# Kernel tuning notes

Hardware: AMD Instinct MI355X
Metric: run time of the kernel (lower is better)

The kernel has to match this reference:

```python
import jax, jax.numpy as jnp
import numpy as np

B, NPG, A, E = 128, 512, 8, 504   # graphs, nodes/graph, agents, edges/graph
F_IN, HID, H = 3, 64, 8
C = HID
F = H * C                          # 512 = concat head output
OUT = 2
NEG_SLOPE = 0.2


def _seg_softmax(alpha, dst, n):
    # edge-softmax normalized over destination-node neighborhoods
    m = jax.ops.segment_max(alpha, dst, num_segments=n)
    e = jnp.exp(alpha - m[dst])
    s = jax.ops.segment_sum(e, dst, num_segments=n)
    return e / jnp.clip(s[dst], 1e-16)


def _gat(x, src, dst, ea, W, b, a_s, a_d, We, a_e, n, self_loops):
    # PyG GATConv: heads=H, concat=True, edge_dim=1, fill_value='mean'
    xs = (x @ W).reshape(n, H, C)                      # [N,H,C]
    als = jnp.einsum('nhc,hc->nh', xs, a_s)            # alpha_src per node
    ald = jnp.einsum('nhc,hc->nh', xs, a_d)            # alpha_dst per node
    if self_loops:
        # fill_value='mean': self-loop attr = mean of incoming edge attrs
        ssum = jax.ops.segment_sum(ea, dst, num_segments=n)
        cnt = jax.ops.segment_sum(jnp.ones((dst.shape[0], 1), ea.dtype), dst, num_segments=n)
        loop_attr = ssum / jnp.maximum(cnt, 1.0)
        ea = jnp.concatenate([ea, loop_attr], axis=0)
        loop = jnp.arange(n, dtype=src.dtype)
        src = jnp.concatenate([src, loop])
        dst = jnp.concatenate([dst, loop])
    ee = (ea @ We).reshape(-1, H, C)                   # lin_edge
    ale = jnp.einsum('ehc,hc->eh', ee, a_e)            # alpha_edge per edge
    alpha = jax.nn.leaky_relu(als[src] + ald[dst] + ale, NEG_SLOPE)  # [E,H]
    alpha = _seg_softmax(alpha, dst, n)
    out = jax.ops.segment_sum(alpha[:, :, None] * xs[src], dst, num_segments=n)
    return out.reshape(n, H * C) + b


def _forward(x, edge_index, edge_attr, p1, p2, p3, fc1_w, fc1_b, fc2_w, fc2_b):
    Bq, npg, _ = x.shape
    n = Bq * npg
    off = (jnp.arange(Bq, dtype=edge_index.dtype) * npg)[:, None]   # PyG Batch offsets
    src = (edge_index[..., 0] + off).reshape(-1)
    dst = (edge_index[..., 1] + off).reshape(-1)
    ea = edge_attr.reshape(-1, 1)
    h = x.reshape(n, -1)
    h = jax.nn.relu(_gat(h, src, dst, ea, *p1, n, False))   # conv1: add_self_loops=False
    h = jax.nn.relu(_gat(h, src, dst, ea, *p2, n, True))
    h = jax.nn.relu(_gat(h, src, dst, ea, *p3, n, True))
    hg = h.reshape(Bq, npg, F)
    graph_emb = hg.mean(axis=1)                      # global_mean_pool (equal-size graphs)
    agent_emb = hg[:, :A].reshape(Bq * A, F)         # first num_agents nodes per graph
    comb = jnp.concatenate([agent_emb, jnp.repeat(graph_emb, A, axis=0)], axis=1)
    comb = jax.nn.relu(comb @ fc1_w + fc1_b)         # fc1 ReLU (extra torch.relu is idempotent)
    pred = comb @ fc2_w + fc2_b
    return pred.reshape(Bq, A, OUT)


def setup_inputs() -> dict:
    key = jax.random.key(0)
    ks = jax.random.split(key, 32)
    rn = lambda i, shape: jax.random.normal(ks[i], shape, jnp.float32) * 0.05
    inp = {
        'x': jax.random.normal(ks[0], (B, NPG, F_IN), jnp.float32),
        'edge_index': jax.random.randint(ks[1], (B, E, 2), 0, NPG, jnp.int32),
        'edge_attr': jax.random.normal(ks[2], (B, E, 1), jnp.float32),
    }
    dims = [F_IN, F, F]
    for li, din in enumerate(dims, start=1):
        inp[f'W{li}'] = rn(3 + li * 6, (din, H * C))
        inp[f'b{li}'] = jnp.zeros((H * C,), jnp.float32)
        inp[f'as{li}'] = rn(4 + li * 6, (H, C))
        inp[f'ad{li}'] = rn(5 + li * 6, (H, C))
        inp[f'We{li}'] = rn(6 + li * 6, (1, H * C))
        inp[f'ae{li}'] = rn(7 + li * 6, (H, C))
    inp['fc1_w'] = rn(28, (2 * F, 4 * HID))
    inp['fc1_b'] = jnp.zeros((4 * HID,), jnp.float32)
    inp['fc2_w'] = rn(29, (4 * HID, OUT))
    inp['fc2_b'] = jnp.zeros((OUT,), jnp.float32)
    return inp


def reference(x, edge_index, edge_attr,
              W1, b1, as1, ad1, We1, ae1,
              W2, b2, as2, ad2, We2, ae2,
              W3, b3, as3, ad3, We3, ae3,
              fc1_w, fc1_b, fc2_w, fc2_b):
    p1 = (W1, b1, as1, ad1, We1, ae1)
    p2 = (W2, b2, as2, ad2, We2, ae2)
    p3 = (W3, b3, as3, ad3, We3, ae3)
    return _forward(x, edge_index, edge_attr, p1, p2, p3, fc1_w, fc1_b, fc2_w, fc2_b)
```

## Files before the change

kernel.cpp:

```cpp
#include <hip/hip_runtime.h>
#include <hip/hip_bf16.h>
#include <math.h>

#define NGRAPH 128
#define NPG_   512
#define NN     (NGRAPH*NPG_)
#define EPG    504
#define ETOT   (NGRAPH*EPG)
#define HEADS  8
#define FDIM   512
#define NEG    0.2f

typedef __hip_bfloat16 bf16;
typedef __attribute__((ext_vector_type(8))) short short8;
typedef __attribute__((ext_vector_type(4))) float f32x4;

static __device__ __forceinline__ float bf(short s){
  union { unsigned u; float f; } c; c.u = ((unsigned)(unsigned short)s) << 16; return c.f;
}
static __device__ __forceinline__ short fbf(float v){
  bf16 b = __float2bfloat16(v); return *(short*)&b;
}

static __device__ __forceinline__ void gload16(void* lds, const void* g){
  __builtin_amdgcn_global_load_lds((const __attribute__((address_space(1))) void*)g,
                                   (__attribute__((address_space(3))) void*)lds, 16, 0, 0);
}

__global__ void k_sentinel(float* out, int n){
  int i = blockIdx.x*blockDim.x + threadIdx.x;
  if (i < n) out[i] = 12345.0f;
}

__global__ __launch_bounds__(512) void k_csr(const int* __restrict__ ei, const float* __restrict__ ea,
                                             const float* __restrict__ We0, const float* __restrict__ ae0,
                                             const float* __restrict__ We1, const float* __restrict__ ae1,
                                             const float* __restrict__ We2, const float* __restrict__ ae2,
                                             const float* __restrict__ W1,
                                             const float* __restrict__ as1, const float* __restrict__ ad1,
                                             int* __restrict__ deg_g, int* __restrict__ row_ptr,
                                             float* __restrict__ la,
                                             int* __restrict__ esrc, float* __restrict__ eattr,
                                             float* __restrict__ coef, float* __restrict__ wsd){
  int b = blockIdx.x;
  int t = threadIdx.x;
  if (b >= NGRAPH){
    if (b < NGRAPH+3){
      int l = b - NGRAPH;
      const float* We = l==0 ? We0 : (l==1 ? We1 : We2);
      const float* ae = l==0 ? ae0 : (l==1 ? ae1 : ae2);
      float v = We[t]*ae[t];
      #pragma unroll
      for (int o=32;o>0;o>>=1) v += __shfl_down(v, o);
      if ((t & 63) == 0) coef[l*HEADS + (t>>6)] = v;
      return;
    }
    float as_v = as1[t], ad_v = ad1[t];
    float v[6] = { W1[t]*as_v, W1[512+t]*as_v, W1[1024+t]*as_v,
                   W1[t]*ad_v, W1[512+t]*ad_v, W1[1024+t]*ad_v };
    #pragma unroll
    for (int o=32;o>0;o>>=1){
      #pragma unroll
      for (int q=0;q<6;q++) v[q] += __shfl_down(v[q], o);
    }
    if ((t & 63) == 0){
      int w = t >> 6;
      wsd[w*3+0]    = v[0]; wsd[w*3+1]    = v[1]; wsd[w*3+2]    = v[2];
      wsd[24+w*3+0] = v[3]; wsd[24+w*3+1] = v[4]; wsd[24+w*3+2] = v[5];
    }
    return;
  }
  __shared__ int   dg[512];
  __shared__ float ss[512];
  __shared__ int   scan[512];
  __shared__ int   cur[512];
  dg[t] = 0; ss[t] = 0.f;
  __syncthreads();
  int src=0, dst=0; float at=0.f;
  if (t < EPG){
    src = ei[(b*EPG+t)*2];
    dst = ei[(b*EPG+t)*2+1];
    at  = ea[b*EPG+t];
    atomicAdd(&dg[dst], 1);
    atomicAdd(&ss[dst], at);
  }
  __syncthreads();
  int d = dg[t];
  scan[t] = d;
  __syncthreads();
  for (int o=1;o<512;o<<=1){
    int v2 = (t>=o) ? scan[t-o] : 0;
    __syncthreads();
    scan[t] += v2;
    __syncthreads();
  }
  int excl = scan[t] - d;
  int n = b*NPG_ + t;
  row_ptr[n] = b*EPG + excl;
  deg_g[n]   = d;
  la[n]      = ss[t] / fmaxf((float)d, 1.f);
  cur[t] = excl;
  __syncthreads();
  if (t < EPG){
    int slot = atomicAdd(&cur[dst], 1);
    int p = b*EPG + slot;
    esrc[p]  = b*NPG_ + src;
    eattr[p] = at;
  }
}

__global__ void k_wt(const float* __restrict__ W1, const float* __restrict__ W2,
                     bf16* __restrict__ wt){
  int idx = blockIdx.x*blockDim.x + threadIdx.x;
  if (idx >= 2*FDIM*FDIM) return;
  int l = idx >> 18;
  int r = idx & (FDIM*FDIM-1);
  int n = r >> 9, k = r & 511;
  const float* W = l ? W2 : W1;
  wt[idx] = __float2bfloat16(W[k*FDIM + n]);
}

__global__ __launch_bounds__(256) void k_gat1(const float* __restrict__ x,
                                              const float* __restrict__ W,
                                              const float* __restrict__ wsd,
                                              const float* __restrict__ coef,
                                              const int* __restrict__ row_ptr,
                                              const int* __restrict__ deg,
                                              const int* __restrict__ esrc,
                                              const float* __restrict__ eattr,
                                              const float* __restrict__ bias,
                                              bf16* __restrict__ h){
  int nwg = gridDim.x;
  int cpx = nwg >> 3;
  int bid = blockIdx.x;
  int swz = (bid & 7)*cpx + (bid >> 3);
  int n = swz*4 + (threadIdx.x >> 6);
  int lane = threadIdx.x & 63;
  int hh = lane >> 3;
  int f0 = lane << 3;

  float ws0 = wsd[hh*3+0],    ws1 = wsd[hh*3+1],    ws2 = wsd[hh*3+2];
  float wd0 = wsd[24+hh*3+0], wd1 = wsd[24+hh*3+1], wd2 = wsd[24+hh*3+2];
  float ch = coef[hh];

  const float* xr = x + n*3;
  float aldn = xr[0]*wd0 + xr[1]*wd1 + xr[2]*wd2;

  int row = row_ptr[n], d = deg[n];
  float m = -1e30f, ssum = 0.f;
  float a0 = 0.f, a1 = 0.f, a2 = 0.f;
  for (int i=0;i<d;i++){
    int s = esrc[row+i]; float at = eattr[row+i];
    const float* xsr = x + s*3;
    float y0 = xsr[0], y1 = xsr[1], y2 = xsr[2];
    float raw = y0*ws0 + y1*ws1 + y2*ws2 + aldn + at*ch;
    raw = raw > 0.f ? raw : NEG*raw;
    float mn = fmaxf(m, raw);
    float sc = __expf(m - mn);
    float p  = __expf(raw - mn);
    ssum = ssum*sc + p;
    a0 = a0*sc + p*y0;
    a1 = a1*sc + p*y1;
    a2 = a2*sc + p*y2;
    m = mn;
  }
  float inv = 1.f / fmaxf(ssum, 1e-16f);
  a0 *= inv; a1 *= inv; a2 *= inv;

  float w0[8], w1[8], w2[8], b8[8];
  #pragma unroll
  for (int j=0;j<8;j+=4){
    *(float4*)&w0[j] = *(const float4*)&W[f0+j];
    *(float4*)&w1[j] = *(const float4*)&W[FDIM+f0+j];
    *(float4*)&w2[j] = *(const float4*)&W[2*FDIM+f0+j];
    *(float4*)&b8[j] = *(const float4*)&bias[f0+j];
  }
  short8 r;
  #pragma unroll
  for (int j=0;j<8;j++){
    float o = a0*w0[j] + a1*w1[j] + a2*w2[j] + b8[j];
    r[j] = fbf(o > 0.f ? o : 0.f);
  }
  ((short8*)(h + (size_t)n*FDIM))[lane] = r;
}

__global__ __launch_bounds__(256) void k_attn_node(const bf16* __restrict__ xs,
                                                   const float* __restrict__ a_s,
                                                   const float* __restrict__ a_d,
                                                   float* __restrict__ als,
                                                   float* __restrict__ ald){
  int n = blockIdx.x*4 + (threadIdx.x >> 6);
  int lane = threadIdx.x & 63;
  short8 v = ((const short8*)(xs + (size_t)n*FDIM))[lane];
  const float4* as4 = (const float4*)a_s;
  const float4* ad4 = (const float4*)a_d;
  float4 sa = as4[lane*2], sb = as4[lane*2+1];
  float4 da = ad4[lane*2], db = ad4[lane*2+1];
  float s = bf(v[0])*sa.x + bf(v[1])*sa.y + bf(v[2])*sa.z + bf(v[3])*sa.w
          + bf(v[4])*sb.x + bf(v[5])*sb.y + bf(v[6])*sb.z + bf(v[7])*sb.w;
  float d = bf(v[0])*da.x + bf(v[1])*da.y + bf(v[2])*da.z + bf(v[3])*da.w
          + bf(v[4])*db.x + bf(v[5])*db.y + bf(v[6])*db.z + bf(v[7])*db.w;
  #pragma unroll
  for (int o=1;o<8;o<<=1){ s += __shfl_xor(s, o); d += __shfl_xor(d, o); }
  if ((lane & 7) == 0){
    int hh = lane >> 3;
    als[n*HEADS+hh] = s;
    ald[n*HEADS+hh] = d;
  }
}

__global__ __launch_bounds__(256) void k_gat(const bf16* __restrict__ xs,
                                             const float* __restrict__ als,
                                             const float* __restrict__ ald,
                                             const float* __restrict__ coef,
                                             const int* __restrict__ row_ptr,
                                             const int* __restrict__ deg,
                                             const int* __restrict__ esrc,
                                             const float* __restrict__ eattr,
                                             const float* __restrict__ la,
                                             const float* __restrict__ bias,
                                             bf16* __restrict__ h){
  int nwg = gridDim.x;
  int cpx = nwg >> 3;
  int bid = blockIdx.x;
  int swz = (bid & 7)*cpx + (bid >> 3);
  int n = swz*4 + (threadIdx.x >> 6);
  int lane = threadIdx.x & 63;
  int hh = lane >> 3;
  int row = row_ptr[n], d = deg[n];
  int tot = d + 1;
  float aldn = ald[n*HEADS+hh];
  float ch = coef[hh];
  float lan = la[n];

  float m = -1e30f, ssum = 0.f;
  float acc[8] = {};
  for (int i=0;i<tot;i++){
    int s; float at;
    if (i<d){ s = esrc[row+i]; at = eattr[row+i]; }
    else    { s = n;           at = lan; }
    float raw = als[s*HEADS+hh] + aldn + at*ch;
    raw = raw > 0.f ? raw : NEG*raw;
    float mn = fmaxf(m, raw);
    float scale = __expf(m - mn);
    float p = __expf(raw - mn);
    ssum = ssum*scale + p;
    short8 v = ((const short8*)(xs + (size_t)s*FDIM))[lane];
    #pragma unroll
    for (int j=0;j<8;j++) acc[j] = acc[j]*scale + p*bf(v[j]);
    m = mn;
  }
  float inv = 1.f / fmaxf(ssum, 1e-16f);
  const float4* b4 = (const float4*)bias;
  float4 ba = b4[lane*2], bb = b4[lane*2+1];
  float bias8[8] = {ba.x,ba.y,ba.z,ba.w,bb.x,bb.y,bb.z,bb.w};
  short8 r;
  #pragma unroll
  for (int j=0;j<8;j++){
    float o = acc[j]*inv + bias8[j];
    r[j] = fbf(o > 0.f ? o : 0.f);
  }
  ((short8*)(h + (size_t)n*FDIM))[lane] = r;
}

__global__ __launch_bounds__(256) void gemm_mfma(const bf16* __restrict__ A,
                                                 const bf16* __restrict__ Wt,
                                                 bf16* __restrict__ C,
                                                 int M, int N, int K){
  __shared__ short As[128*64];
  __shared__ short Bs[128*64];
  int bid = blockIdx.x;
  int wk = ((bid & 7) << 8) | (bid >> 3);
  const int bm = (wk >> 2)*128, bn = (wk & 3)*128;
  const int tid = threadIdx.x;
  const int lane = tid & 63;
  const int w = tid >> 6;
  const int wm = (w >> 1)*64, wn = (w & 1)*64;
  const int lr = lane & 15;
  const int lk = lane >> 4;

  f32x4 acc[4][4] = {};

  for (int k0 = 0; k0 < K; k0 += 64){
    #pragma unroll
    for (int is = 0; is < 4; ++is){
      int i = is*256 + tid;
      int r = i >> 3, g = i & 7;
      int gs = g ^ (r & 7);
      gload16(&As[i*8], A  + (size_t)(bm+r)*K + k0 + gs*8);
      gload16(&Bs[i*8], Wt + (size_t)(bn+r)*K + k0 + gs*8);
    }
    __syncthreads();
    #pragma unroll
    for (int kk = 0; kk < 2; ++kk){
      short8 af[4], bfr[4];
      #pragma unroll
      for (int mi=0; mi<4; ++mi){
        int row = wm + mi*16 + lr;
        int g = (kk*4 + lk) ^ (row & 7);
        af[mi] = *(const short8*)&As[row*64 + g*8];
      }
      #pragma unroll
      for (int ni=0; ni<4; ++ni){
        int row = wn + ni*16 + lr;
        int g = (kk*4 + lk) ^ (row & 7);
        bfr[ni] = *(const short8*)&Bs[row*64 + g*8];
      }
      #pragma unroll
      for (int mi=0; mi<4; ++mi)
        #pragma unroll
        for (int ni=0; ni<4; ++ni)
          acc[mi][ni] = __builtin_amdgcn_mfma_f32_16x16x32_bf16(af[mi], bfr[ni], acc[mi][ni], 0,0,0);
    }
    __syncthreads();
  }

  #pragma unroll
  for (int mi=0; mi<4; ++mi)
    #pragma unroll
    for (int ni=0; ni<4; ++ni){
      int col = bn + wn + ni*16 + lr;
      #pragma unroll
      for (int r=0; r<4; ++r){
        int rowg = bm + wm + mi*16 + lk*4 + r;
        C[(size_t)rowg*N + col] = __float2bfloat16(acc[mi][ni][r]);
      }
    }
}

__global__ __launch_bounds__(256) void k_gemb1(const bf16* __restrict__ h, float* __restrict__ pgemb){
  int gs_ = blockIdx.x;
  int g = gs_ >> 3, s = gs_ & 7;
  int t = threadIdx.x;
  int c = t & 63, rg = t >> 6;
  const bf16* base = h + ((size_t)(g*NPG_ + s*64 + rg*16))*FDIM;
  float acc[8] = {};
  #pragma unroll 4
  for (int i=0;i<16;i++){
    short8 v = ((const short8*)(base + (size_t)i*FDIM))[c];
    #pragma unroll
    for (int j=0;j<8;j++) acc[j] += bf(v[j]);
  }
  float* dst = pgemb + ((size_t)(gs_*4 + rg))*FDIM + c*8;
  float4 lo = {acc[0],acc[1],acc[2],acc[3]};
  float4 hi = {acc[4],acc[5],acc[6],acc[7]};
  *(float4*)dst = lo;
  *(float4*)(dst+4) = hi;
}

__global__ __launch_bounds__(1024) void k_head(const bf16* __restrict__ h,
                                               const float* __restrict__ pgemb,
                                               const float* __restrict__ fc1w,
                                               const float* __restrict__ fc1b,
                                               const float* __restrict__ fc2w,
                                               const float* __restrict__ fc2b,
                                               float* __restrict__ out){
  __shared__ float ge[FDIM];
  __shared__ float ag[8][FDIM];
  __shared__ float ps[2][8][257];
  __shared__ float gs2[2][256];
  __shared__ float f1[8][256];
  int g = blockIdx.x, t = threadIdx.x;

  if (t < FDIM){
    float s = 0.f;
    const float* p = pgemb + (size_t)g*32*FDIM + t;
    #pragma unroll
    for (int c=0;c<32;c++) s += p[(size_t)c*FDIM];
    ge[t] = s * (1.f/NPG_);
  } else {
    int i = t - FDIM;
    int r = i >> 6, c = i & 63;
    short8 v = ((const short8*)(h + (size_t)(g*NPG_ + r)*FDIM))[c];
    #pragma unroll
    for (int j=0;j<8;j++) ag[r][c*8+j] = bf(v[j]);
  }
  __syncthreads();

  int col = t & 255, q = t >> 8;
  if (q < 2){
    float acc[8] = {};
    int kbeg = q*256;
    for (int k = kbeg; k < kbeg+256; k += 4){
      float w0 = fc1w[(k+0)*256+col];
      float w1 = fc1w[(k+1)*256+col];
      float w2 = fc1w[(k+2)*256+col];
      float w3 = fc1w[(k+3)*256+col];
      #pragma unroll
      for (int r=0;r<8;r++){
        float4 a = *(const float4*)&ag[r][k];
        acc[r] += a.x*w0 + a.y*w1 + a.z*w2 + a.w*w3;
      }
    }
    #pragma unroll
    for (int r=0;r<8;r++) ps[q][r][col] = acc[r];
  } else {
    float gacc = 0.f;
    int kbeg = (q-2)*256;
    for (int k = kbeg; k < kbeg+256; k += 4){
      float v0 = fc1w[(FDIM+k+0)*256+col];
      float v1 = fc1w[(FDIM+k+1)*256+col];
      float v2 = fc1w[(FDIM+k+2)*256+col];
      float v3 = fc1w[(FDIM+k+3)*256+col];
      float4 gv = *(const float4*)&ge[k];
      gacc += gv.x*v0 + gv.y*v1 + gv.z*v2 + gv.w*v3;
    }
    gs2[q-2][col] = gacc;
  }
  __syncthreads();

  if (t < 256){
    float b = fc1b[t] + gs2[0][t] + gs2[1][t];
    #pragma unroll
    for (int r=0;r<8;r++)
      f1[r][t] = fmaxf(ps[0][r][t] + ps[1][r][t] + b, 0.f);
  }
  __syncthreads();

  if (t < 128){
    int r = t >> 4, o = (t >> 3) & 1, l = t & 7;
    float s = 0.f;
    for (int k = l; k < 256; k += 8) s += f1[r][k] * fc2w[k*2+o];
    #pragma unroll
    for (int off=4; off; off>>=1) s += __shfl_down(s, off);
    if (l == 0) out[(g*8 + r)*2 + o] = s + fc2b[o];
  }
}

extern "C" void kernel_launch(void* const* d_in, const int* in_sizes, int n_in,
                              void* d_out, int out_size, void* d_ws, size_t ws_size,
                              hipStream_t stream)
{
  const float* x    = (const float*)d_in[0];
  const int*   ei   = (const int*)  d_in[1];
  const float* ea   = (const float*)d_in[2];
  const float* Wl[3]  = {(const float*)d_in[3],  (const float*)d_in[9],  (const float*)d_in[15]};
  const float* Bl[3]  = {(const float*)d_in[4],  (const float*)d_in[10], (const float*)d_in[16]};
  const float* ASl[3] = {(const float*)d_in[5],  (const float*)d_in[11], (const float*)d_in[17]};
  const float* ADl[3] = {(const float*)d_in[6],  (const float*)d_in[12], (const float*)d_in[18]};
  const float* WEl[3] = {(const float*)d_in[7],  (const float*)d_in[13], (const float*)d_in[19]};
  const float* AEl[3] = {(const float*)d_in[8],  (const float*)d_in[14], (const float*)d_in[20]};
  const float* FC1W = (const float*)d_in[21];
  const float* FC1B = (const float*)d_in[22];
  const float* FC2W = (const float*)d_in[23];
  const float* FC2B = (const float*)d_in[24];
  float* out = (float*)d_out;
  (void)in_sizes; (void)n_in;

  char* ws = (char*)d_ws;
  size_t off = 0;
  auto alloc = [&](size_t bytes)->char*{
    char* p = ws + off;
    off = (off + bytes + 255) & ~(size_t)255;
    return p;
  };
  bf16*  h       = (bf16*) alloc((size_t)NN*FDIM*2);
  bf16*  xs      = (bf16*) alloc((size_t)NN*FDIM*2);
  float* als     = (float*)alloc((size_t)NN*HEADS*4);
  float* ald     = (float*)alloc((size_t)NN*HEADS*4);
  float* la      = (float*)alloc((size_t)NN*4);
  int*   deg     = (int*)  alloc((size_t)NN*4);
  int*   row_ptr = (int*)  alloc((size_t)NN*4);
  int*   esrc    = (int*)  alloc((size_t)ETOT*4);
  float* eattr   = (float*)alloc((size_t)ETOT*4);
  float* coef    = (float*)alloc(3*HEADS*4);
  float* wsd     = (float*)alloc(48*4);
  bf16*  wt      = (bf16*) alloc((size_t)2*FDIM*FDIM*2);
  float* pgemb   = (float*)alloc((size_t)NGRAPH*32*FDIM*4);

  if (off > ws_size){
    k_sentinel<<<(out_size+255)/256, 256, 0, stream>>>(out, out_size);
    return;
  }

  k_csr<<<NGRAPH+4, 512, 0, stream>>>(ei, ea, WEl[0], AEl[0], WEl[1], AEl[1], WEl[2], AEl[2],
                                      Wl[0], ASl[0], ADl[0],
                                      deg, row_ptr, la, esrc, eattr, coef, wsd);
  k_wt<<<(2*FDIM*FDIM+255)/256, 256, 0, stream>>>(Wl[1], Wl[2], wt);

  k_gat1<<<NN/4, 256, 0, stream>>>(x, Wl[0], wsd, coef, row_ptr, deg, esrc, eattr, Bl[0], h);

  for (int l=1;l<3;l++){
    gemm_mfma<<<2048, 256, 0, stream>>>(h, wt + (size_t)(l-1)*FDIM*FDIM, xs, NN, FDIM, FDIM);
    k_attn_node<<<NN/4, 256, 0, stream>>>(xs, ASl[l], ADl[l], als, ald);
    k_gat<<<NN/4, 256, 0, stream>>>(xs, als, ald, coef + l*HEADS, row_ptr, deg, esrc, eattr, la, Bl[l], h);
  }

  k_gemb1<<<NGRAPH*8, 256, 0, stream>>>(h, pgemb);
  k_head <<<NGRAPH, 1024, 0, stream>>>(h, pgemb, FC1W, FC1B, FC2W, FC2B, out);
}
```

Before: 255.1 us.

## Fuse attention-score projection into GEMM epilogue and split head over K

The per-node attention dot products (alpha_src/alpha_dst) are now computed inside the MFMA GEMM epilogue from fp32 accumulators, which removes the separate k_attn_node kernel and its re-read of xs. Each 64-column wave tile maps to one head, so the reduction is a 16-lane shuffle. The readout head is split into a K-parallel k_head1 over 1024 blocks that writes partial sums, followed by a small k_fc2 reduction. This exposes more parallelism than 128 large blocks, at the cost of extra workspace traffic and a slightly different rounding (fp32 instead of bf16 xs for the scores).

```diff
diff --git a/kernel.cpp b/kernel.cpp
--- a/kernel.cpp
+++ b/kernel.cpp
@@ -182,31 +182,6 @@
     r[j] = fbf(o > 0.f ? o : 0.f);
   }
   ((short8*)(h + (size_t)n*FDIM))[lane] = r;
-}
-
-__global__ __launch_bounds__(256) void k_attn_node(const bf16* __restrict__ xs,
-                                                   const float* __restrict__ a_s,
-                                                   const float* __restrict__ a_d,
-                                                   float* __restrict__ als,
-                                                   float* __restrict__ ald){
-  int n = blockIdx.x*4 + (threadIdx.x >> 6);
-  int lane = threadIdx.x & 63;
-  short8 v = ((const short8*)(xs + (size_t)n*FDIM))[lane];
-  const float4* as4 = (const float4*)a_s;
-  const float4* ad4 = (const float4*)a_d;
-  float4 sa = as4[lane*2], sb = as4[lane*2+1];
-  float4 da = ad4[lane*2], db = ad4[lane*2+1];
-  float s = bf(v[0])*sa.x + bf(v[1])*sa.y + bf(v[2])*sa.z + bf(v[3])*sa.w
-          + bf(v[4])*sb.x + bf(v[5])*sb.y + bf(v[6])*sb.z + bf(v[7])*sb.w;
-  float d = bf(v[0])*da.x + bf(v[1])*da.y + bf(v[2])*da.z + bf(v[3])*da.w
-          + bf(v[4])*db.x + bf(v[5])*db.y + bf(v[6])*db.z + bf(v[7])*db.w;
-  #pragma unroll
-  for (int o=1;o<8;o<<=1){ s += __shfl_xor(s, o); d += __shfl_xor(d, o); }
-  if ((lane & 7) == 0){
-    int hh = lane >> 3;
-    als[n*HEADS+hh] = s;
-    ald[n*HEADS+hh] = d;
-  }
 }
 
 __global__ __launch_bounds__(256) void k_gat(const bf16* __restrict__ xs,
@@ -265,7 +240,11 @@
 
 __global__ __launch_bounds__(256) void gemm_mfma(const bf16* __restrict__ A,
                                                  const bf16* __restrict__ Wt,
+                                                 const float* __restrict__ a_s,
+                                                 const float* __restrict__ a_d,
                                                  bf16* __restrict__ C,
+                                                 float* __restrict__ als,
+                                                 float* __restrict__ ald,
                                                  int M, int N, int K){
   __shared__ short As[128*64];
   __shared__ short Bs[128*64];
@@ -315,6 +294,31 @@
     __syncthreads();
   }
 
+  int hh = (bn + wn) >> 6;
+  float as_c[4], ad_c[4];
+  #pragma unroll
+  for (int ni=0; ni<4; ++ni){
+    int c = hh*64 + ni*16 + lr;
+    as_c[ni] = a_s[c];
+    ad_c[ni] = a_d[c];
+  }
+  #pragma unroll
+  for (int mi=0; mi<4; ++mi)
+    #pragma unroll
+    for (int r=0; r<4; ++r){
+      float s = acc[mi][0][r]*as_c[0] + acc[mi][1][r]*as_c[1]
+              + acc[mi][2][r]*as_c[2] + acc[mi][3][r]*as_c[3];
+      float d = acc[mi][0][r]*ad_c[0] + acc[mi][1][r]*ad_c[1]
+              + acc[mi][2][r]*ad_c[2] + acc[mi][3][r]*ad_c[3];
+      #pragma unroll
+      for (int o=1;o<16;o<<=1){ s += __shfl_xor(s, o); d += __shfl_xor(d, o); }
+      if (lr == 0){
+        int rowg = bm + wm + mi*16 + lk*4 + r;
+        als[rowg*HEADS+hh] = s;
+        ald[rowg*HEADS+hh] = d;
+      }
+    }
+
   #pragma unroll
   for (int mi=0; mi<4; ++mi)
     #pragma unroll
@@ -348,75 +352,67 @@
   *(float4*)(dst+4) = hi;
 }
 
-__global__ __launch_bounds__(1024) void k_head(const bf16* __restrict__ h,
+__global__ __launch_bounds__(256) void k_head1(const bf16* __restrict__ h,
                                                const float* __restrict__ pgemb,
                                                const float* __restrict__ fc1w,
-                                               const float* __restrict__ fc1b,
-                                               const float* __restrict__ fc2w,
-                                               const float* __restrict__ fc2b,
-                                               float* __restrict__ out){
-  __shared__ float ge[FDIM];
-  __shared__ float ag[8][FDIM];
-  __shared__ float ps[2][8][257];
-  __shared__ float gs2[2][256];
+                                               float* __restrict__ pf1,
+                                               float* __restrict__ pge){
+  __shared__ float ge[64];
+  __shared__ float ag[8][64];
+  int blk = blockIdx.x;
+  int g = blk >> 3, q = blk & 7;
+  int t = threadIdx.x;
+  int k0 = q*64;
+
+  if (t < 64){
+    float s = 0.f;
+    const float* p = pgemb + ((size_t)g*32)*FDIM + k0 + t;
+    #pragma unroll 8
+    for (int c=0;c<32;c++) s += p[(size_t)c*FDIM];
+    ge[t] = s * (1.f/NPG_);
+  } else if (t < 128){
+    int i = t - 64;
+    int r = i >> 3, c8 = i & 7;
+    short8 v = ((const short8*)(h + ((size_t)(g*NPG_ + r))*FDIM + k0))[c8];
+    #pragma unroll
+    for (int j=0;j<8;j++) ag[r][c8*8+j] = bf(v[j]);
+  }
+  __syncthreads();
+
+  float acc[8] = {};
+  float gacc = 0.f;
+  for (int kk=0; kk<64; kk++){
+    float wa = fc1w[(size_t)(k0+kk)*256 + t];
+    float wg = fc1w[(size_t)(FDIM+k0+kk)*256 + t];
+    #pragma unroll
+    for (int r=0;r<8;r++) acc[r] += ag[r][kk]*wa;
+    gacc += ge[kk]*wg;
+  }
+  #pragma unroll
+  for (int r=0;r<8;r++) pf1[((size_t)q*1024 + g*8 + r)*256 + t] = acc[r];
+  pge[((size_t)q*NGRAPH + g)*256 + t] = gacc;
+}
+
+__global__ __launch_bounds__(256) void k_fc2(const float* __restrict__ pf1,
+                                             const float* __restrict__ pge,
+                                             const float* __restrict__ fc1b,
+                                             const float* __restrict__ fc2w,
+                                             const float* __restrict__ fc2b,
+                                             float* __restrict__ out){
   __shared__ float f1[8][256];
   int g = blockIdx.x, t = threadIdx.x;
-
-  if (t < FDIM){
+  float ges = 0.f;
+  #pragma unroll
+  for (int q=0;q<8;q++) ges += pge[((size_t)q*NGRAPH + g)*256 + t];
+  float b = fc1b[t] + ges;
+  #pragma unroll
+  for (int r=0;r<8;r++){
     float s = 0.f;
-    const float* p = pgemb + (size_t)g*32*FDIM + t;
-    #pragma unroll
-    for (int c=0;c<32;c++) s += p[(size_t)c*FDIM];
-    ge[t] = s * (1.f/NPG_);
-  } else {
-    int i = t - FDIM;
-    int r = i >> 6, c = i & 63;
-    short8 v = ((const short8*)(h + (size_t)(g*NPG_ + r)*FDIM))[c];
-    #pragma unroll
-    for (int j=0;j<8;j++) ag[r][c*8+j] = bf(v[j]);
-  }
-  __syncthreads();
-
-  int col = t & 255, q = t >> 8;
-  if (q < 2){
-    float acc[8] = {};
-    int kbeg = q*256;
-    for (int k = kbeg; k < kbeg+256; k += 4){
-      float w0 = fc1w[(k+0)*256+col];
-      float w1 = fc1w[(k+1)*256+col];
-      float w2 = fc1w[(k+2)*256+col];
-      float w3 = fc1w[(k+3)*256+col];
-      #pragma unroll
-      for (int r=0;r<8;r++){
-        float4 a = *(const float4*)&ag[r][k];
-        acc[r] += a.x*w0 + a.y*w1 + a.z*w2 + a.w*w3;
-      }
-    }
-    #pragma unroll
-    for (int r=0;r<8;r++) ps[q][r][col] = acc[r];
-  } else {
-    float gacc = 0.f;
-    int kbeg = (q-2)*256;
-    for (int k = kbeg; k < kbeg+256; k += 4){
-      float v0 = fc1w[(FDIM+k+0)*256+col];
-      float v1 = fc1w[(FDIM+k+1)*256+col];
-      float v2 = fc1w[(FDIM+k+2)*256+col];
-      float v3 = fc1w[(FDIM+k+3)*256+col];
-      float4 gv = *(const float4*)&ge[k];
-      gacc += gv.x*v0 + gv.y*v1 + gv.z*v2 + gv.w*v3;
-    }
-    gs2[q-2][col] = gacc;
-  }
-  __syncthreads();
-
-  if (t < 256){
-    float b = fc1b[t] + gs2[0][t] + gs2[1][t];
-    #pragma unroll
-    for (int r=0;r<8;r++)
-      f1[r][t] = fmaxf(ps[0][r][t] + ps[1][r][t] + b, 0.f);
-  }
-  __syncthreads();
-
+    #pragma unroll
+    for (int q=0;q<8;q++) s += pf1[((size_t)q*1024 + g*8 + r)*256 + t];
+    f1[r][t] = fmaxf(s + b, 0.f);
+  }
+  __syncthreads();
   if (t < 128){
     int r = t >> 4, o = (t >> 3) & 1, l = t & 7;
     float s = 0.f;
@@ -467,6 +463,8 @@
   float* wsd     = (float*)alloc(48*4);
   bf16*  wt      = (bf16*) alloc((size_t)2*FDIM*FDIM*2);
   float* pgemb   = (float*)alloc((size_t)NGRAPH*32*FDIM*4);
+  float* pf1     = (float*)alloc((size_t)8*1024*256*4);
+  float* pge     = (float*)alloc((size_t)8*NGRAPH*256*4);
 
   if (off > ws_size){
     k_sentinel<<<(out_size+255)/256, 256, 0, stream>>>(out, out_size);
@@ -481,11 +479,12 @@
   k_gat1<<<NN/4, 256, 0, stream>>>(x, Wl[0], wsd, coef, row_ptr, deg, esrc, eattr, Bl[0], h);
 
   for (int l=1;l<3;l++){
-    gemm_mfma<<<2048, 256, 0, stream>>>(h, wt + (size_t)(l-1)*FDIM*FDIM, xs, NN, FDIM, FDIM);
-    k_attn_node<<<NN/4, 256, 0, stream>>>(xs, ASl[l], ADl[l], als, ald);
+    gemm_mfma<<<2048, 256, 0, stream>>>(h, wt + (size_t)(l-1)*FDIM*FDIM,
+                                        ASl[l], ADl[l], xs, als, ald, NN, FDIM, FDIM);
     k_gat<<<NN/4, 256, 0, stream>>>(xs, als, ald, coef + l*HEADS, row_ptr, deg, esrc, eattr, la, Bl[l], h);
   }
 
   k_gemb1<<<NGRAPH*8, 256, 0, stream>>>(h, pgemb);
-  k_head <<<NGRAPH, 1024, 0, stream>>>(h, pgemb, FC1W, FC1B, FC2W, FC2B, out);
-}
+  k_head1<<<NGRAPH*8, 256, 0, stream>>>(h, pgemb, FC1W, pf1, pge);
+  k_fc2 <<<NGRAPH, 256, 0, stream>>>(pf1, pge, FC1B, FC2W, FC2B, out);
+}
```

Result: faster. 240.7 us (-5.7%).
